# Kernel optimization log

Hardware: AMD Instinct MI355X
Metric: run time of the kernel (lower is better)

The kernel has to match this reference:

```python
import jax, jax.numpy as jnp
import numpy as np

HEADS = 8
DIM_HEAD = 64


def setup_inputs() -> dict:
    key = jax.random.key(0)
    ks = jax.random.split(key, 5)
    B, N, C, coor = 2, 2048, 256, 3
    dim_inner = HEADS * DIM_HEAD  # 512
    # weight scale 1/16 ~ 1/sqrt(256) keeps softmax logits in a sane range
    w_scale = 1.0 / 16.0
    return {
        "x": jax.random.normal(ks[0], (B, N, C, coor), dtype=jnp.float32),
        "Wq": jax.random.normal(ks[1], (dim_inner, C), dtype=jnp.float32) * w_scale,
        "Wk": jax.random.normal(ks[2], (dim_inner, C), dtype=jnp.float32) * w_scale,
        "Wv": jax.random.normal(ks[3], (dim_inner, C), dtype=jnp.float32) * w_scale,
        "Wo": jax.random.normal(ks[4], (C, dim_inner), dtype=jnp.float32) * w_scale,
    }


def _split_heads(t, B, N, coor):
    # b n (h d) c -> b h n (d c)
    t = t.reshape(B, N, HEADS, DIM_HEAD, coor)
    t = t.transpose(0, 2, 1, 3, 4)
    return t.reshape(B, HEADS, N, DIM_HEAD * coor)


def reference(x, Wq, Wk, Wv, Wo):
    B, N, C, coor = x.shape
    # VNLinear: einsum('... i c, o i -> ... o c')
    q = jnp.einsum('bnic,oi->bnoc', x, Wq)
    k = jnp.einsum('bnic,oi->bnoc', x, Wk)
    v = jnp.einsum('bnic,oi->bnoc', x, Wv)
    q = _split_heads(q, B, N, coor)  # (B, H, N, d*c)
    k = _split_heads(k, B, N, coor)
    v = _split_heads(v, B, N, coor)
    scale = (DIM_HEAD * coor) ** -0.5
    sim = jnp.einsum('bhie,bhje->bhij', q, k) * scale  # (B, H, N, N)
    attn = jax.nn.softmax(sim, axis=-1)
    out = jnp.einsum('bhij,bhje->bhie', attn, v)  # (B, H, N, d*c)
    # b h n (d c) -> b n (h d) c
    out = out.reshape(B, HEADS, N, DIM_HEAD, coor).transpose(0, 2, 1, 3, 4)
    out = out.reshape(B, N, HEADS * DIM_HEAD, coor)
    # to_out VNLinear
    return jnp.einsum('bnic,oi->bnoc', out, Wo)  # (B, N, C, 3)
```

## Files before the change

### kernel.cpp

```cpp
#include <hip/hip_runtime.h>

#define HEADS 8
#define DH 64
#define CO 3
#define E 192
#define NSEQ 2048
#define BATCH 2
#define CIN 256
#define DINNER 512
#define NTOK 4096
#define BHTOT 16

typedef __attribute__((ext_vector_type(8))) short bf16x8;
typedef __attribute__((ext_vector_type(4))) short bf16x4;
typedef __attribute__((ext_vector_type(4))) float f32x4;
typedef __attribute__((ext_vector_type(4))) float float4v;

static __device__ inline short f2bf(float f) {
  union { float f; unsigned u; } v; v.f = f;
  unsigned r = (v.u + 0x7FFFu + ((v.u >> 16) & 1u)) >> 16;
  return (short)r;
}

static __device__ inline float bf2f(short s) {
  union { unsigned u; float f; } a;
  a.u = ((unsigned)(unsigned short)s) << 16;
  return a.f;
}

static __device__ inline void load_lds16(const short* g, short* l) {
  __builtin_amdgcn_global_load_lds(
      (const __attribute__((address_space(1))) void*)g,
      (__attribute__((address_space(3))) void*)l, 16, 0, 0);
}


__global__ __launch_bounds__(256) void prep(const float* __restrict__ x,
                                            const float* __restrict__ Wq,
                                            const float* __restrict__ Wk,
                                            const float* __restrict__ Wv,
                                            const float* __restrict__ Wo,
                                            short* __restrict__ xcp,
                                            short* __restrict__ wqkvp,
                                            short* __restrict__ wop) {
  int tid = threadIdx.x;
  if (blockIdx.x < 256) {
    __shared__ short st[12288];
    int mt = blockIdx.x;
    const float* xb = x + (size_t)mt * 12288;
#pragma unroll
    for (int r = 0; r < 12; r++) {
      int idx4 = r * 256 + tid;
      float4v v = *(const float4v*)(xb + idx4 * 4);
#pragma unroll
      for (int e = 0; e < 4; e++) {
        int fp = idx4 * 4 + e;
        int ti = fp / 3, c = fp - ti * 3;
        int tl = ti >> 8, i = ti & 255;
        int ks = i >> 5, qd = (i >> 3) & 3, j = i & 7;
        st[c * 4096 + ks * 512 + (qd * 16 + tl) * 8 + j] = f2bf(v[e]);
      }
    }
    __syncthreads();
    short* dst = xcp;
#pragma unroll
    for (int rep = 0; rep < 6; rep++) {
      int g = rep * 256 + tid;
      int c = g >> 9, rem = g & 511;
      *(bf16x8*)(dst + ((size_t)(c * 256 + mt) * 8) * 512 + rem * 8) =
          *(const bf16x8*)&st[c * 4096 + rem * 8];
    }
    return;
  }
  int idx = (blockIdx.x - 256) * 256 + tid;
  const float qscale = 0.07216878364870323f * 1.4426950408889634f;
  if (idx < 1536 * 256) {
    int o = idx >> 8, i = idx & 255;
    float v;
    if (o < 512) v = Wq[idx] * qscale;
    else if (o < 1024) v = Wk[idx - 512 * 256];
    else v = Wv[idx - 1024 * 256];
    int nt = o >> 4, ln = o & 15, ks = i >> 5, qd = (i >> 3) & 3, j = i & 7;
    wqkvp[((size_t)(nt * 8 + ks)) * 512 + (qd * 16 + ln) * 8 + j] = f2bf(v);
  } else {
    int j0 = idx - 1536 * 256;
    if (j0 < 256 * 512) {
      int o2 = j0 >> 9, i = j0 & 511;
      int nt = o2 >> 4, ln = o2 & 15, ks = i >> 5, qd = (i >> 3) & 3, j = i & 7;
      wop[((size_t)(nt * 16 + ks)) * 512 + (qd * 16 + ln) * 8 + j] = f2bf(Wo[j0]);
    }
  }
}

__global__ __launch_bounds__(256, 4) void qkv_gemm(const short* __restrict__ xcp,
                                                   const short* __restrict__ wqkvp,
                                                   short* __restrict__ qp,
                                                   short* __restrict__ kp,
                                                   short* __restrict__ vp) {
  __shared__ __align__(16) short pool[9216];
  int c = blockIdx.z, ntb = blockIdx.x, mtb = blockIdx.y;
  int tid = threadIdx.x, wave = tid >> 6, lane = tid & 63;
  int ln = lane & 15, quad = lane >> 4;
  int wm = wave >> 1, wn = wave & 1;

  const short* gA = xcp + ((size_t)(c * 256 + mtb * 8) * 8) * 512;

  f32x4 acc[4][2] = {};
#pragma unroll
  for (int i = 0; i < 2; i++) {
    int q = tid + 256 * i, mf = q >> 6, l = q & 63;
    load_lds16(gA + (size_t)(mf * 8) * 512 + l * 8, pool + q * 8);
  }
  for (int ks = 0; ks < 8; ks++) {
    int b = ks & 1;
    __syncthreads();
    if (ks < 7) {
#pragma unroll
      for (int i = 0; i < 2; i++) {
        int q = tid + 256 * i, mf = q >> 6, l = q & 63;
        load_lds16(gA + (size_t)(mf * 8 + ks + 1) * 512 + l * 8,
                   pool + (b ^ 1) * 4096 + q * 8);
      }
    }
    const short* As = pool + b * 4096;
    bf16x8 af[4], bfr[2];
#pragma unroll
    for (int j = 0; j < 2; j++)
      bfr[j] = *(const bf16x8*)(wqkvp +
          (size_t)((ntb * 4 + wn * 2 + j) * 8 + ks) * 512 + lane * 8);
#pragma unroll
    for (int i = 0; i < 4; i++) af[i] = *(const bf16x8*)&As[(wm * 4 + i) * 512 + lane * 8];
#pragma unroll
    for (int i = 0; i < 4; i++)
#pragma unroll
      for (int j = 0; j < 2; j++)
        acc[i][j] = __builtin_amdgcn_mfma_f32_16x16x32_bf16(af[i], bfr[j], acc[i][j], 0, 0, 0);
  }

  int mat = ntb >> 3;
  int h = ntb & 7;
  int b0 = mtb >> 4;
  int bhx = b0 * 8 + h;
  if (mat < 2) {
    __syncthreads();
    short* tp = pool;
#pragma unroll
    for (int i = 0; i < 4; i++)
#pragma unroll
      for (int j = 0; j < 2; j++)
#pragma unroll
        for (int jj = 0; jj < 4; jj++)
          tp[(wm * 64 + i * 16 + quad * 4 + jj) * 72 + wn * 32 + j * 16 + ln] =
              f2bf(acc[i][j][jj]);
    __syncthreads();
    short* dst = (mat == 0) ? qp : kp;
#pragma unroll
    for (int rep = 0; rep < 4; rep++) {
      int gi = rep * 256 + tid;
      int l2 = gi & 15, qd = (gi >> 4) & 3, nf2 = (gi >> 6) & 3,
          esp = (gi >> 8) & 1, kt2 = (gi >> 9) & 1;
      int tl = kt2 * 64 + nf2 * 16 + l2;
      bf16x8 val = *(const bf16x8*)&tp[tl * 72 + esp * 32 + qd * 8];
      int kt = (mtb * 2 + kt2) & 31;
      int es = c * 2 + esp;
      size_t off = (((size_t)((bhx * 32 + kt) * 24) + es * 4 + nf2) * 64 +
                    (size_t)(qd * 16 + l2)) * 8;
      *(bf16x8*)(dst + off) = val;
    }
  } else {
#pragma unroll
    for (int i = 0; i < 4; i++) {
      int kt = (mtb * 2 + wm) & 31;
      int ks2 = (i >> 1) & 1;
      int qd2 = (i * 2 + (quad >> 1)) & 3;
#pragma unroll
      for (int j = 0; j < 2; j++) {
        int ef = c * 4 + wn * 2 + j;
        size_t off = ((size_t)((bhx * 32 + kt) * 24 + ks2 * 12 + ef)) * 512 +
                     (qd2 * 16 + ln) * 8 + (quad & 1) * 4;
        bf16x4 val = { f2bf(acc[i][j][0]), f2bf(acc[i][j][1]),
                       f2bf(acc[i][j][2]), f2bf(acc[i][j][3]) };
        *(bf16x4*)(vp + off) = val;
      }
    }
  }
}

__global__ __launch_bounds__(256, 2) void attn(const short* __restrict__ qp,
                                               const short* __restrict__ kp,
                                               const short* __restrict__ vp,
                                               short* __restrict__ opart,
                                               float* __restrict__ lpart) {
  __shared__ __align__(16) short pool[29696];
  int pair = blockIdx.x, qt = blockIdx.y;
  int bh = pair & 15, kh = pair >> 4;
  int tid = threadIdx.x, wave = tid >> 6, lane = tid & 63;
  int ln = lane & 15, quad = lane >> 4;
  short* Pl = pool + 24576;

  bf16x8 qf[2][6];
#pragma unroll
  for (int rg = 0; rg < 2; rg++) {
    int fi = wave * 2 + rg;
    const short* qb = qp +
        ((size_t)(bh * 32 + qt * 2 + (fi >> 2)) * 24 + (fi & 3)) * 512 + lane * 8;
#pragma unroll
    for (int es = 0; es < 6; es++) qf[rg][es] = *(const bf16x8*)(qb + es * 2048);
  }

  float l_r[2][4] = {};
  f32x4 acc[2][12] = {};
  const short* gKb = kp + (size_t)(bh * 32 + kh * 16) * 12288;
  const short* gVb = vp + (size_t)(bh * 32 + kh * 16) * 12288;

  auto stage = [&](int k32, int buf) {
    const short* g64K = gKb + (size_t)(k32 >> 1) * 12288;
    const short* g64V = gVb + (size_t)(k32 >> 1) * 12288;
    int half = k32 & 1;
    short* Kd = pool + buf * 6144;
    short* Vd = pool + 12288 + buf * 6144;
#pragma unroll
    for (int i = 0; i < 3; i++) {
      int q = i * 256 + tid;
      int f = q >> 6, l = q & 63;
      int es = f >> 1, nfl = f & 1;
      load_lds16(g64K + (size_t)(es * 4 + half * 2 + nfl) * 512 + l * 8, Kd + q * 8);
      load_lds16(g64V + (size_t)(half * 12 + f) * 512 + l * 8, Vd + q * 8);
    }
  };

  stage(0, 0);
  for (int kt = 0; kt < 32; kt++) {
    int b = kt & 1;
    __syncthreads();
    if (kt < 31) stage(kt + 1, b ^ 1);
    const short* Kl = pool + b * 6144;
    const short* Vl = pool + 12288 + b * 6144;

    f32x4 s[2][2] = {};
#pragma unroll
    for (int es = 0; es < 6; es++) {
#pragma unroll
      for (int nfl = 0; nfl < 2; nfl++) {
        bf16x8 kf = *(const bf16x8*)&Kl[(es * 2 + nfl) * 512 + lane * 8];
        s[0][nfl] = __builtin_amdgcn_mfma_f32_16x16x32_bf16(qf[0][es], kf, s[0][nfl], 0, 0, 0);
        s[1][nfl] = __builtin_amdgcn_mfma_f32_16x16x32_bf16(qf[1][es], kf, s[1][nfl], 0, 0, 0);
      }
    }

#pragma unroll
    for (int rg = 0; rg < 2; rg++)
#pragma unroll
      for (int jj = 0; jj < 4; jj++)
#pragma unroll
        for (int nfl = 0; nfl < 2; nfl++) {
          float p = __builtin_amdgcn_exp2f(s[rg][nfl][jj]);
          union { float f; unsigned u; } v; v.f = p;
          Pl[((wave * 2 + rg) * 16 + quad * 4 + jj) * 40 + nfl * 16 + ln] =
              (short)((v.u + 0x8000u) >> 16);
          l_r[rg][jj] += p;
        }

    bf16x8 pa[2];
#pragma unroll
    for (int rg = 0; rg < 2; rg++)
      pa[rg] = *(const bf16x8*)&Pl[((wave * 2 + rg) * 16 + ln) * 40 + quad * 8];

#pragma unroll
    for (int ef = 0; ef < 12; ef++) {
      bf16x8 v0 = *(const bf16x8*)&Vl[ef * 512 + lane * 8];
      acc[0][ef] = __builtin_amdgcn_mfma_f32_16x16x32_bf16(pa[0], v0, acc[0][ef], 0, 0, 0);
      acc[1][ef] = __builtin_amdgcn_mfma_f32_16x16x32_bf16(pa[1], v0, acc[1][ef], 0, 0, 0);
    }
  }

#pragma unroll
  for (int rg = 0; rg < 2; rg++)
#pragma unroll
    for (int jj = 0; jj < 4; jj++)
#pragma unroll
      for (int off = 1; off < 16; off <<= 1)
        l_r[rg][jj] += __shfl_xor(l_r[rg][jj], off, 64);

  __syncthreads();
  short* tp = pool;
#pragma unroll
  for (int rg = 0; rg < 2; rg++)
#pragma unroll
    for (int jj = 0; jj < 4; jj++) {
      int row = (wave * 2 + rg) * 16 + quad * 4 + jj;
#pragma unroll
      for (int ef = 0; ef < 12; ef++)
        tp[row * 200 + ef * 16 + ln] = f2bf(acc[rg][ef][jj]);
    }
  __syncthreads();
  const size_t obase = ((size_t)(kh * 16 + bh) * 2048 + qt * 128) * 192;
#pragma unroll
  for (int rep = 0; rep < 12; rep++) {
    int gi = rep * 256 + tid;
    int row = gi / 24, c8 = gi - row * 24;
    *(bf16x8*)(opart + obase + (size_t)row * 192 + c8 * 8) =
        *(const bf16x8*)&tp[row * 200 + c8 * 8];
  }
  int lb = (kh * 16 + bh) * 2048 + qt * 128;
  if (ln == 0) {
#pragma unroll
    for (int rg = 0; rg < 2; rg++)
#pragma unroll
      for (int jj = 0; jj < 4; jj++)
        lpart[lb + (wave * 2 + rg) * 16 + quad * 4 + jj] = l_r[rg][jj];
  }
}

__global__ __launch_bounds__(256) void out_gemm(const short* __restrict__ opart,
                                                const float* __restrict__ lpart,
                                                const short* __restrict__ wop,
                                                float* __restrict__ out) {
  __shared__ __align__(16) float pool_f[12352];
  short* Al = (short*)pool_f;
  int mtb = blockIdx.x;
  int tid = threadIdx.x, wave = tid >> 6, lane = tid & 63;
  int ln = lane & 15, quad = lane >> 4;
  const size_t HSTR = (size_t)16 * 2048 * 192;

#pragma unroll
  for (int rep = 0; rep < 12; rep++) {
    int g = rep * 256 + tid;
    int c = g >> 10, inner = g & 1023;
    int d8 = inner & 7, h = (inner >> 3) & 7, row16 = inner >> 6;
    int t = mtb * 16 + row16, b = t >> 11, n = t & 2047;
    int bh = b * 8 + h;
    size_t src = ((size_t)bh * 2048 + n) * 192 + c * 64 + d8 * 8;
    bf16x8 o1 = *(const bf16x8*)(opart + src);
    bf16x8 o2 = *(const bf16x8*)(opart + HSTR + src);
    float l = lpart[bh * 2048 + n] + lpart[32768 + bh * 2048 + n];
    float inv = 1.f / l;
    bf16x8 r;
#pragma unroll
    for (int j = 0; j < 8; j++) r[j] = f2bf((bf2f(o1[j]) + bf2f(o2[j])) * inv);
    int ks = h * 2 + (d8 >> 2), qd = d8 & 3;
    *(bf16x8*)&Al[c * 8192 + ks * 512 + (qd * 16 + row16) * 8] = r;
  }
  __syncthreads();

  f32x4 acc[3][4] = {};
  for (int ks = 0; ks < 16; ks++) {
    bf16x8 af[3];
#pragma unroll
    for (int c = 0; c < 3; c++) af[c] = *(const bf16x8*)&Al[c * 8192 + ks * 512 + lane * 8];
#pragma unroll
    for (int jf = 0; jf < 4; jf++) {
      int nt = wave * 4 + jf;
      bf16x8 bfr = *(const bf16x8*)(wop + (size_t)(nt * 16 + ks) * 512 + lane * 8);
#pragma unroll
      for (int c = 0; c < 3; c++)
        acc[c][jf] = __builtin_amdgcn_mfma_f32_16x16x32_bf16(af[c], bfr, acc[c][jf], 0, 0, 0);
    }
  }
  __syncthreads();
#pragma unroll
  for (int c = 0; c < 3; c++)
#pragma unroll
    for (int jf = 0; jf < 4; jf++) {
      int o2 = (wave * 4 + jf) * 16 + ln;
#pragma unroll
      for (int jj = 0; jj < 4; jj++)
        pool_f[(quad * 4 + jj) * 772 + o2 * 3 + c] = acc[c][jf][jj];
    }
  __syncthreads();
  float* ob = out + (size_t)mtb * 12288;
#pragma unroll
  for (int rep = 0; rep < 12; rep++) {
    int idx = rep * 256 + tid;
    int row = idx / 192, col4 = idx - row * 192;
    *(float4v*)(ob + row * 768 + col4 * 4) =
        *(const float4v*)(pool_f + row * 772 + col4 * 4);
  }
}

extern "C" void kernel_launch(void* const* d_in, const int* in_sizes, int n_in,
                              void* d_out, int out_size, void* d_ws, size_t ws_size,
                              hipStream_t stream) {
  const float* x  = (const float*)d_in[0];
  const float* Wq = (const float*)d_in[1];
  const float* Wk = (const float*)d_in[2];
  const float* Wv = (const float*)d_in[3];
  const float* Wo = (const float*)d_in[4];
  float* out = (float*)d_out;

  short* ws    = (short*)d_ws;
  short* xcp   = ws;
  short* wqkvp = xcp + 3 * NTOK * CIN;
  short* wop   = wqkvp + 1536 * 256;
  short* qp    = wop + 256 * 512;
  short* kp    = qp + (size_t)BHTOT * NSEQ * E;
  short* vp    = kp + (size_t)BHTOT * NSEQ * E;
  short* opart = vp + (size_t)BHTOT * NSEQ * E;
  float* lpart = (float*)xcp;

  prep<<<2304, 256, 0, stream>>>(x, Wq, Wk, Wv, Wo, xcp, wqkvp, wop);
  qkv_gemm<<<dim3(24, 32, 3), 256, 0, stream>>>(xcp, wqkvp, qp, kp, vp);
  attn<<<dim3(32, 16), 256, 0, stream>>>(qp, kp, vp, opart, lpart);
  out_gemm<<<256, 256, 0, stream>>>(opart, lpart, wop, out);
}
```

Baseline: 159.5 us.

## Transpose QK^T MFMA operands for packed P stores and stage two k-slices per phase

In the attention kernel, the K and Q operands of the score MFMA are swapped so each lane holds a column of scores for one query row. This lets the exp'd probabilities be written to LDS as packed 4-element vectors instead of scalar shorts, and cuts the row-sum reduction to two cross-quad shuffles per row group. Separately, the QKV GEMM now stages two k-slices per barrier phase with a larger LDS pool, halving the number of syncs. The trade-off is more LDS per block in the QKV GEMM, which may lower its occupancy.

```diff
diff --git a/kernel.cpp b/kernel.cpp
--- a/kernel.cpp
+++ b/kernel.cpp
@@ -97,7 +97,7 @@
                                                    short* __restrict__ qp,
                                                    short* __restrict__ kp,
                                                    short* __restrict__ vp) {
-  __shared__ __align__(16) short pool[9216];
+  __shared__ __align__(16) short pool[16384];
   int c = blockIdx.z, ntb = blockIdx.x, mtb = blockIdx.y;
   int tid = threadIdx.x, wave = tid >> 6, lane = tid & 63;
   int ln = lane & 15, quad = lane >> 4;
@@ -105,36 +105,39 @@
 
   const short* gA = xcp + ((size_t)(c * 256 + mtb * 8) * 8) * 512;
 
+  auto stage = [&](int ph, int buf) {
+#pragma unroll
+    for (int i = 0; i < 4; i++) {
+      int q = i * 256 + tid;
+      int half = q >> 9, mf = (q >> 6) & 7, l = q & 63;
+      load_lds16(gA + (size_t)(mf * 8 + ph * 2 + half) * 512 + l * 8,
+                 pool + buf * 8192 + (q & 511) * 8 + half * 4096);
+    }
+  };
+
   f32x4 acc[4][2] = {};
-#pragma unroll
-  for (int i = 0; i < 2; i++) {
-    int q = tid + 256 * i, mf = q >> 6, l = q & 63;
-    load_lds16(gA + (size_t)(mf * 8) * 512 + l * 8, pool + q * 8);
-  }
-  for (int ks = 0; ks < 8; ks++) {
-    int b = ks & 1;
+  stage(0, 0);
+  for (int ph = 0; ph < 4; ph++) {
+    int b = ph & 1;
     __syncthreads();
-    if (ks < 7) {
-#pragma unroll
-      for (int i = 0; i < 2; i++) {
-        int q = tid + 256 * i, mf = q >> 6, l = q & 63;
-        load_lds16(gA + (size_t)(mf * 8 + ks + 1) * 512 + l * 8,
-                   pool + (b ^ 1) * 4096 + q * 8);
-      }
-    }
-    const short* As = pool + b * 4096;
-    bf16x8 af[4], bfr[2];
-#pragma unroll
-    for (int j = 0; j < 2; j++)
-      bfr[j] = *(const bf16x8*)(wqkvp +
-          (size_t)((ntb * 4 + wn * 2 + j) * 8 + ks) * 512 + lane * 8);
-#pragma unroll
-    for (int i = 0; i < 4; i++) af[i] = *(const bf16x8*)&As[(wm * 4 + i) * 512 + lane * 8];
-#pragma unroll
-    for (int i = 0; i < 4; i++)
+    if (ph < 3) stage(ph + 1, b ^ 1);
+#pragma unroll
+    for (int half = 0; half < 2; half++) {
+      int ks = ph * 2 + half;
+      const short* As = pool + b * 8192 + half * 4096;
+      bf16x8 af[4], bfr[2];
 #pragma unroll
       for (int j = 0; j < 2; j++)
-        acc[i][j] = __builtin_amdgcn_mfma_f32_16x16x32_bf16(af[i], bfr[j], acc[i][j], 0, 0, 0);
+        bfr[j] = *(const bf16x8*)(wqkvp +
+            (size_t)((ntb * 4 + wn * 2 + j) * 8 + ks) * 512 + lane * 8);
+#pragma unroll
+      for (int i = 0; i < 4; i++) af[i] = *(const bf16x8*)&As[(wm * 4 + i) * 512 + lane * 8];
+#pragma unroll
+      for (int i = 0; i < 4; i++)
+#pragma unroll
+        for (int j = 0; j < 2; j++)
+          acc[i][j] = __builtin_amdgcn_mfma_f32_16x16x32_bf16(af[i], bfr[j], acc[i][j], 0, 0, 0);
+    }
   }
 
   int mat = ntb >> 3;
@@ -208,7 +211,7 @@
     for (int es = 0; es < 6; es++) qf[rg][es] = *(const bf16x8*)(qb + es * 2048);
   }
 
-  float l_r[2][4] = {};
+  float l_r[2] = {0.f, 0.f};
   f32x4 acc[2][12] = {};
   const short* gKb = kp + (size_t)(bh * 32 + kh * 16) * 12288;
   const short* gVb = vp + (size_t)(bh * 32 + kh * 16) * 12288;
@@ -243,23 +246,25 @@
 #pragma unroll
       for (int nfl = 0; nfl < 2; nfl++) {
         bf16x8 kf = *(const bf16x8*)&Kl[(es * 2 + nfl) * 512 + lane * 8];
-        s[0][nfl] = __builtin_amdgcn_mfma_f32_16x16x32_bf16(qf[0][es], kf, s[0][nfl], 0, 0, 0);
-        s[1][nfl] = __builtin_amdgcn_mfma_f32_16x16x32_bf16(qf[1][es], kf, s[1][nfl], 0, 0, 0);
+        s[0][nfl] = __builtin_amdgcn_mfma_f32_16x16x32_bf16(kf, qf[0][es], s[0][nfl], 0, 0, 0);
+        s[1][nfl] = __builtin_amdgcn_mfma_f32_16x16x32_bf16(kf, qf[1][es], s[1][nfl], 0, 0, 0);
       }
     }
 
 #pragma unroll
     for (int rg = 0; rg < 2; rg++)
 #pragma unroll
-      for (int jj = 0; jj < 4; jj++)
-#pragma unroll
-        for (int nfl = 0; nfl < 2; nfl++) {
+      for (int nfl = 0; nfl < 2; nfl++) {
+        bf16x4 pk4;
+#pragma unroll
+        for (int jj = 0; jj < 4; jj++) {
           float p = __builtin_amdgcn_exp2f(s[rg][nfl][jj]);
           union { float f; unsigned u; } v; v.f = p;
-          Pl[((wave * 2 + rg) * 16 + quad * 4 + jj) * 40 + nfl * 16 + ln] =
-              (short)((v.u + 0x8000u) >> 16);
-          l_r[rg][jj] += p;
+          pk4[jj] = (short)((v.u + 0x8000u) >> 16);
+          l_r[rg] += p;
         }
+        *(bf16x4*)&Pl[((wave * 2 + rg) * 16 + ln) * 40 + nfl * 16 + quad * 4] = pk4;
+      }
 
     bf16x8 pa[2];
 #pragma unroll
@@ -275,12 +280,10 @@
   }
 
 #pragma unroll
-  for (int rg = 0; rg < 2; rg++)
-#pragma unroll
-    for (int jj = 0; jj < 4; jj++)
-#pragma unroll
-      for (int off = 1; off < 16; off <<= 1)
-        l_r[rg][jj] += __shfl_xor(l_r[rg][jj], off, 64);
+  for (int rg = 0; rg < 2; rg++) {
+    l_r[rg] += __shfl_xor(l_r[rg], 16, 64);
+    l_r[rg] += __shfl_xor(l_r[rg], 32, 64);
+  }
 
   __syncthreads();
   short* tp = pool;
@@ -303,12 +306,10 @@
         *(const bf16x8*)&tp[row * 200 + c8 * 8];
   }
   int lb = (kh * 16 + bh) * 2048 + qt * 128;
-  if (ln == 0) {
+  if (quad == 0) {
 #pragma unroll
     for (int rg = 0; rg < 2; rg++)
-#pragma unroll
-      for (int jj = 0; jj < 4; jj++)
-        lpart[lb + (wave * 2 + rg) * 16 + quad * 4 + jj] = l_r[rg][jj];
+      lpart[lb + (wave * 2 + rg) * 16 + ln] = l_r[rg];
   }
 }
 
```

Measured after the change: 159.9 us. About the same (+0.3%).
